# Kernel tuning notes

Measured on AMD Instinct MI355X. Metric: run time of the kernel, lower is better.

## Reference

```python
import jax, jax.numpy as jnp
import numpy as np

EMBED_DIM = 512
NUM_HEADS = 8
HEAD_DIM = EMBED_DIM // NUM_HEADS


def setup_inputs() -> dict:
    key = jax.random.key(0)
    k1, k2, kw, kb, kow, kob = jax.random.split(key, 6)
    B, L, C = 2, 2048, EMBED_DIM
    s = 1.0 / np.sqrt(C)
    return {
        "x1": jax.random.normal(k1, (B, L, C), dtype=jnp.float32),
        "x2": jax.random.normal(k2, (B, L, C), dtype=jnp.float32),
        # nn.Linear(embed_dim, 3*embed_dim): weight [3C, C], bias [3C]
        "qkv_w": jax.random.uniform(kw, (3 * C, C), jnp.float32, -s, s),
        "qkv_b": jax.random.uniform(kb, (3 * C,), jnp.float32, -s, s),
        # nn.Linear(embed_dim, embed_dim): weight [C, C], bias [C]
        "out_w": jax.random.uniform(kow, (C, C), jnp.float32, -s, s),
        "out_b": jax.random.uniform(kob, (C,), jnp.float32, -s, s),
    }


def _qkv(x, qkv_w, qkv_b):
    B, L, C = x.shape
    H, D = NUM_HEADS, C // NUM_HEADS
    # Linear: x @ W^T + b, then view(B, L, H, 3, D) and split along the '3' axis
    qkv = (jnp.einsum("blc,fc->blf", x, qkv_w) + qkv_b).reshape(B, L, H, 3, D)
    qkv = jnp.transpose(qkv, (3, 0, 2, 1, 4))  # [3, B, H, L, D]
    return qkv[0], qkv[1], qkv[2]


def _attend(q, k, v):
    # q,k,v: [B, H, L, D]; scale by 1/sqrt(D)
    scale = 1.0 / np.sqrt(q.shape[-1]).astype(np.float32)
    scores = jnp.einsum("bhqd,bhkd->bhqk", q, k) * scale  # [B,H,L,L]
    attn = jax.nn.softmax(scores, axis=-1)
    out = jnp.einsum("bhqk,bhkd->bhqd", attn, v)
    B, H, L, D = out.shape
    return jnp.transpose(out, (0, 2, 1, 3)).reshape(B, L, H * D)


def reference(x1, x2, qkv_w, qkv_b, out_w, out_b):
    q1, k1, v1 = _qkv(x1, qkv_w, qkv_b)
    q2, k2, v2 = _qkv(x2, qkv_w, qkv_b)
    out1 = _attend(q1, k2, v2)  # q from x1, k/v from x2
    out2 = _attend(q2, k1, v1)  # q from x2, k/v from x1
    out1 = jnp.einsum("blc,fc->blf", out1, out_w) + out_b
    out2 = jnp.einsum("blc,fc->blf", out2, out_w) + out_b
    return (out1, out2)
```

## Files before the change

kernel.cpp:

```cpp
#include <hip/hip_runtime.h>
#include <stdint.h>

typedef unsigned short u16;
typedef unsigned int u32;
typedef short bf16x8 __attribute__((ext_vector_type(8)));
typedef float f32x4 __attribute__((ext_vector_type(4)));
typedef float f32x16 __attribute__((ext_vector_type(16)));

#define K_DIM 512

__device__ __forceinline__ u16 f2bf(float f) {
  union { float f; u32 u; } v; v.f = f;
  return (u16)((v.u + 0x8000u) >> 16);
}
__device__ __forceinline__ u32 pk2(float lo, float hi) {
  union { float f; u32 u; } a, b; a.f = lo; b.f = hi;
  return __builtin_amdgcn_perm(b.u + 0x8000u, a.u + 0x8000u, 0x07060302u);
}

__global__ void cvt_kernel(const float* __restrict__ x1, const float* __restrict__ x2,
                           const float* __restrict__ qkvw, const float* __restrict__ outw,
                           u16* __restrict__ xb, u16* __restrict__ wqkv, u16* __restrict__ wout) {
  int tid = blockIdx.x * 256 + threadIdx.x;
  const float4* src; u16* dst; int idx = tid;
  if (idx < 524288)        { src = (const float4*)x1;   dst = xb; }
  else if (idx < 1048576)  { src = (const float4*)x2;   dst = xb + 2097152; idx -= 524288; }
  else if (idx < 1245184)  { src = (const float4*)qkvw; dst = wqkv;         idx -= 1048576; }
  else                     { src = (const float4*)outw; dst = wout;         idx -= 1245184; }
  float4 v = src[idx];
  *(uint2*)&dst[idx * 4] = make_uint2(pk2(v.x, v.y), pk2(v.z, v.w));
}

#define LDA 40

__global__ __launch_bounds__(256, 3) void qkv_gemm(
    const u16* __restrict__ A, const u16* __restrict__ W, const float* __restrict__ bias,
    u16* __restrict__ qb, u16* __restrict__ kb, u16* __restrict__ vtb) {
  __shared__ __align__(16) u16 As[2][128 * LDA];
  __shared__ __align__(16) u16 Bs[2][128 * LDA];
  const int t = threadIdx.x;
  const int m0 = blockIdx.x * 128, n0 = blockIdx.y * 128;
  const int lane = t & 63, l16 = lane & 15, quad = lane >> 4;
  const int w = t >> 6;
  const int wm = (w >> 1) * 64, wn = (w & 1) * 64;
  const int sr = t >> 2, sc = (t & 3) * 8;

  const u16* Ap = A + (size_t)(m0 + sr) * K_DIM + sc;
  const u16* Wp = W + (size_t)(n0 + sr) * K_DIM + sc;

  f32x4 acc[4][4];
#pragma unroll
  for (int i = 0; i < 4; ++i)
#pragma unroll
    for (int j = 0; j < 4; ++j) acc[i][j] = (f32x4){0.f, 0.f, 0.f, 0.f};

  uint4 ra0 = *(const uint4*)(Ap);
  uint4 ra1 = *(const uint4*)(Ap + 64 * K_DIM);
  uint4 rb0 = *(const uint4*)(Wp);
  uint4 rb1 = *(const uint4*)(Wp + 64 * K_DIM);
  *(uint4*)&As[0][sr * LDA + sc] = ra0;
  *(uint4*)&As[0][(sr + 64) * LDA + sc] = ra1;
  *(uint4*)&Bs[0][sr * LDA + sc] = rb0;
  *(uint4*)&Bs[0][(sr + 64) * LDA + sc] = rb1;
  ra0 = *(const uint4*)(Ap + 32);
  ra1 = *(const uint4*)(Ap + 64 * K_DIM + 32);
  rb0 = *(const uint4*)(Wp + 32);
  rb1 = *(const uint4*)(Wp + 64 * K_DIM + 32);
  __syncthreads();

  for (int kt = 0; kt < 16; ++kt) {
    const int cur = kt & 1, nxt = cur ^ 1;
    if (kt < 15) {
      *(uint4*)&As[nxt][sr * LDA + sc] = ra0;
      *(uint4*)&As[nxt][(sr + 64) * LDA + sc] = ra1;
      *(uint4*)&Bs[nxt][sr * LDA + sc] = rb0;
      *(uint4*)&Bs[nxt][(sr + 64) * LDA + sc] = rb1;
    }
    if (kt < 14) {
      int ko = (kt + 2) * 32;
      ra0 = *(const uint4*)(Ap + ko);
      ra1 = *(const uint4*)(Ap + 64 * K_DIM + ko);
      rb0 = *(const uint4*)(Wp + ko);
      rb1 = *(const uint4*)(Wp + 64 * K_DIM + ko);
    }
    bf16x8 af[4], bfr[4];
#pragma unroll
    for (int mi = 0; mi < 4; ++mi)
      af[mi] = *(const bf16x8*)&As[cur][(wm + mi * 16 + l16) * LDA + quad * 8];
#pragma unroll
    for (int ni = 0; ni < 4; ++ni)
      bfr[ni] = *(const bf16x8*)&Bs[cur][(wn + ni * 16 + l16) * LDA + quad * 8];
#pragma unroll
    for (int mi = 0; mi < 4; ++mi)
#pragma unroll
      for (int ni = 0; ni < 4; ++ni)
        acc[mi][ni] = __builtin_amdgcn_mfma_f32_16x16x32_bf16(bfr[ni], af[mi], acc[mi][ni], 0, 0, 0);
    __syncthreads();
  }

  const int fbase = n0 + wn;
  const int h = fbase / 192;
  const int s = (fbase - h * 192) >> 6;
  float4 bv[4];
#pragma unroll
  for (int ni = 0; ni < 4; ++ni)
    bv[ni] = *(const float4*)&bias[fbase + ni * 16 + quad * 4];
  const int bh = m0 >> 11;
  const int lbase = (m0 & 2047) + wm;

  if (s == 2) {
    u16* dst = vtb + (size_t)((bh * 8 + h) * 64) * 2048;
#pragma unroll
    for (int mi = 0; mi < 4; ++mi) {
      int l = lbase + mi * 16 + l16;
#pragma unroll
      for (int ni = 0; ni < 4; ++ni)
#pragma unroll
        for (int r = 0; r < 4; ++r)
          dst[(ni * 16 + quad * 4 + r) * 2048 + l] = f2bf(acc[mi][ni][r] + bv[ni][r]);
    }
  } else {
    u16* dst = (s == 0 ? qb : kb) + (size_t)((bh * 8 + h) * 2048) * 64;
    const float sc2 = (s == 0) ? 0.18033688011112042f : 1.0f;
#pragma unroll
    for (int mi = 0; mi < 4; ++mi) {
      int l = lbase + mi * 16 + l16;
#pragma unroll
      for (int ni = 0; ni < 4; ++ni) {
        float v0 = (acc[mi][ni][0] + bv[ni][0]) * sc2;
        float v1 = (acc[mi][ni][1] + bv[ni][1]) * sc2;
        float v2 = (acc[mi][ni][2] + bv[ni][2]) * sc2;
        float v3 = (acc[mi][ni][3] + bv[ni][3]) * sc2;
        *(uint2*)&dst[(size_t)l * 64 + ni * 16 + quad * 4] = make_uint2(pk2(v0, v1), pk2(v2, v3));
      }
    }
  }
}

#define LQ 72

#define SPHASE(SS, KBUF)                                                          \
  do {                                                                            \
    _Pragma("unroll") for (int r_ = 0; r_ < 16; ++r_) {                           \
      SS[0][r_] = 0.f; SS[1][r_] = 0.f;                                           \
    }                                                                             \
    _Pragma("unroll") for (int ks_ = 0; ks_ < 4; ++ks_) {                         \
      bf16x8 kfr0 = *(const bf16x8*)&Ks[KBUF][l32 * LQ + ks_ * 16 + h2 * 8];      \
      bf16x8 kfr1 = *(const bf16x8*)&Ks[KBUF][(32 + l32) * LQ + ks_ * 16 + h2 * 8]; \
      SS[0] = __builtin_amdgcn_mfma_f32_32x32x16_bf16(kfr0, qf[ks_], SS[0], 0, 0, 0); \
      SS[1] = __builtin_amdgcn_mfma_f32_32x32x16_bf16(kfr1, qf[ks_], SS[1], 0, 0, 0); \
    }                                                                             \
  } while (0)

#define SOFTPV(SS, VBUF)                                                          \
  do {                                                                            \
    bf16x8 pf[4];                                                                 \
    _Pragma("unroll") for (int mi_ = 0; mi_ < 2; ++mi_) {                         \
      float p[16];                                                                \
      _Pragma("unroll") for (int r_ = 0; r_ < 16; ++r_)                           \
        p[r_] = __builtin_amdgcn_exp2f(SS[mi_][r_]);                              \
      _Pragma("unroll") for (int r_ = 0; r_ < 16; r_ += 4)                        \
        rs += (p[r_] + p[r_ + 1]) + (p[r_ + 2] + p[r_ + 3]);                      \
      u32 a0 = pk2(p[0], p[1]),   b0 = pk2(p[2], p[3]);                           \
      u32 c0 = pk2(p[4], p[5]),   d0 = pk2(p[6], p[7]);                           \
      u32 a1 = pk2(p[8], p[9]),   b1 = pk2(p[10], p[11]);                         \
      u32 c1 = pk2(p[12], p[13]), d1 = pk2(p[14], p[15]);                         \
      asm("v_permlane32_swap_b32 %0, %1" : "+v"(a0), "+v"(c0));                   \
      asm("v_permlane32_swap_b32 %0, %1" : "+v"(b0), "+v"(d0));                   \
      asm("v_permlane32_swap_b32 %0, %1" : "+v"(a1), "+v"(c1));                   \
      asm("v_permlane32_swap_b32 %0, %1" : "+v"(b1), "+v"(d1));                   \
      union { u32 u[4]; bf16x8 v; } f0_, f1_;                                     \
      f0_.u[0] = a0; f0_.u[1] = b0; f0_.u[2] = c0; f0_.u[3] = d0;                 \
      f1_.u[0] = a1; f1_.u[1] = b1; f1_.u[2] = c1; f1_.u[3] = d1;                 \
      pf[mi_ * 2] = f0_.v; pf[mi_ * 2 + 1] = f1_.v;                               \
    }                                                                             \
    const u16* vb_ = (const u16*)VTs + (VBUF) * (64 * LQ);                        \
    _Pragma("unroll") for (int ks_ = 0; ks_ < 4; ++ks_) {                         \
      bf16x8 vf0 = *(const bf16x8*)&vb_[l32 * LQ + ks_ * 16 + h2 * 8];            \
      bf16x8 vf1 = *(const bf16x8*)&vb_[(32 + l32) * LQ + ks_ * 16 + h2 * 8];     \
      oacc[0] = __builtin_amdgcn_mfma_f32_32x32x16_bf16(vf0, pf[ks_], oacc[0], 0, 0, 0); \
      oacc[1] = __builtin_amdgcn_mfma_f32_32x32x16_bf16(vf1, pf[ks_], oacc[1], 0, 0, 0); \
    }                                                                             \
  } while (0)

__global__ __launch_bounds__(256, 2) void attn_kernel(
    const u16* __restrict__ qb, const u16* __restrict__ kb, const u16* __restrict__ vtb,
    u16* __restrict__ attnb) {
  __shared__ __align__(16) u16 Ks[2][64 * LQ];
  __shared__ __align__(16) u16 VTs[4][64 * LQ];

  const int t = threadIdx.x;
  const int w = t >> 6, lane = t & 63, l32 = lane & 31, h2 = lane >> 5;
  const int bid = blockIdx.x;
  const int comb = bid & 31;
  const int qt = bid >> 5;
  const int h = comb & 7, bb = (comb >> 3) & 1, pair = comb >> 4;
  const int in_q = pair, in_kv = pair ^ 1;

  const u16* Qg = qb + (size_t)((in_q * 2 + bb) * 8 + h) * 2048 * 64;
  const u16* Kg = kb + (size_t)((in_kv * 2 + bb) * 8 + h) * 2048 * 64;
  const u16* Vg = vtb + (size_t)((in_kv * 2 + bb) * 8 + h) * 64 * 2048;

  const int srow = t >> 3, sseg = (t & 7) * 8;
  uint4 rk0 = *(const uint4*)(Kg + srow * 64 + sseg);
  uint4 rk1 = *(const uint4*)(Kg + (srow + 32) * 64 + sseg);
  uint4 rv0 = *(const uint4*)(Vg + srow * 2048 + sseg);
  uint4 rv1 = *(const uint4*)(Vg + (srow + 32) * 2048 + sseg);

  bf16x8 qf[4];
#pragma unroll
  for (int ks = 0; ks < 4; ++ks)
    qf[ks] = *(const bf16x8*)(Qg + (qt * 128 + w * 32 + l32) * 64 + ks * 16 + h2 * 8);

  auto stage = [&](int kbuf, int vbuf) {
    *(uint4*)&Ks[kbuf][srow * LQ + sseg] = rk0;
    *(uint4*)&Ks[kbuf][(srow + 32) * LQ + sseg] = rk1;
    *(uint4*)&VTs[vbuf][srow * LQ + sseg] = rv0;
    *(uint4*)&VTs[vbuf][(srow + 32) * LQ + sseg] = rv1;
  };
  auto gload = [&](int kt) {
    const int ko = kt * 64;
    rk0 = *(const uint4*)(Kg + (ko + srow) * 64 + sseg);
    rk1 = *(const uint4*)(Kg + (ko + srow + 32) * 64 + sseg);
    rv0 = *(const uint4*)(Vg + srow * 2048 + ko + sseg);
    rv1 = *(const uint4*)(Vg + (srow + 32) * 2048 + ko + sseg);
  };

  f32x16 oacc[2];
#pragma unroll
  for (int mi = 0; mi < 2; ++mi)
#pragma unroll
    for (int r = 0; r < 16; ++r) oacc[mi][r] = 0.f;
  float rs = 0.f;
  f32x16 sA[2], sB[2];

  stage(0, 0);
  gload(1);
  __syncthreads();

  SPHASE(sA, 0);
  stage(1, 1);
  gload(2);
  __syncthreads();

#pragma unroll 1
  for (int it = 0; it < 16; ++it) {
    const int e = (it & 1) << 1;
    SPHASE(sB, 1);
    SOFTPV(sA, e);
    if (it == 15) break;
    stage(0, e ^ 2);
    gload(2 * it + 3);
    __syncthreads();
    SPHASE(sA, 0);
    SOFTPV(sB, e + 1);
    stage(1, e ^ 3);
    if (it < 14) gload(2 * it + 4);
    __syncthreads();
  }
  SOFTPV(sB, 3);

  rs += __shfl_xor(rs, 32);
  const float inv = 1.0f / rs;
  const int row = in_q * 4096 + bb * 2048 + qt * 128 + w * 32 + l32;
#pragma unroll
  for (int mi = 0; mi < 2; ++mi)
#pragma unroll
    for (int rg = 0; rg < 4; ++rg) {
      float v0 = oacc[mi][rg * 4 + 0] * inv;
      float v1 = oacc[mi][rg * 4 + 1] * inv;
      float v2 = oacc[mi][rg * 4 + 2] * inv;
      float v3 = oacc[mi][rg * 4 + 3] * inv;
      *(uint2*)&attnb[(size_t)row * 512 + h * 64 + mi * 32 + rg * 8 + h2 * 4] =
          make_uint2(pk2(v0, v1), pk2(v2, v3));
    }
}

__global__ __launch_bounds__(256, 2) void out_gemm(
    const u16* __restrict__ A, const u16* __restrict__ W, const float* __restrict__ bias,
    float* __restrict__ out) {
  __shared__ __align__(16) u16 As[2][64 * LDA];
  __shared__ __align__(16) u16 Bs[2][128 * LDA];
  const int t = threadIdx.x;
  const int m0 = blockIdx.x * 64, n0 = blockIdx.y * 128;
  const int lane = t & 63, l16 = lane & 15, quad = lane >> 4;
  const int w = t >> 6;
  const int wm = (w & 1) * 32, wn = (w >> 1) * 64;
  const int ar = t >> 2, ac = (t & 3) * 8;
  const int sr = t >> 2, sc = (t & 3) * 8;

  const u16* Ap = A + (size_t)(m0 + ar) * K_DIM + ac;
  const u16* Wp = W + (size_t)(n0 + sr) * K_DIM + sc;

  f32x4 acc[2][4];
#pragma unroll
  for (int i = 0; i < 2; ++i)
#pragma unroll
    for (int j = 0; j < 4; ++j) acc[i][j] = (f32x4){0.f, 0.f, 0.f, 0.f};

  uint4 ra = *(const uint4*)Ap;
  uint4 rb0 = *(const uint4*)(Wp);
  uint4 rb1 = *(const uint4*)(Wp + 64 * K_DIM);
  *(uint4*)&As[0][ar * LDA + ac] = ra;
  *(uint4*)&Bs[0][sr * LDA + sc] = rb0;
  *(uint4*)&Bs[0][(sr + 64) * LDA + sc] = rb1;
  ra = *(const uint4*)(Ap + 32);
  rb0 = *(const uint4*)(Wp + 32);
  rb1 = *(const uint4*)(Wp + 64 * K_DIM + 32);
  __syncthreads();

  for (int kt = 0; kt < 16; ++kt) {
    const int cur = kt & 1, nxt = cur ^ 1;
    if (kt < 15) {
      *(uint4*)&As[nxt][ar * LDA + ac] = ra;
      *(uint4*)&Bs[nxt][sr * LDA + sc] = rb0;
      *(uint4*)&Bs[nxt][(sr + 64) * LDA + sc] = rb1;
    }
    if (kt < 14) {
      int ko = (kt + 2) * 32;
      ra = *(const uint4*)(Ap + ko);
      rb0 = *(const uint4*)(Wp + ko);
      rb1 = *(const uint4*)(Wp + 64 * K_DIM + ko);
    }
    bf16x8 af[2], bfr[4];
#pragma unroll
    for (int mi = 0; mi < 2; ++mi)
      af[mi] = *(const bf16x8*)&As[cur][(wm + mi * 16 + l16) * LDA + quad * 8];
#pragma unroll
    for (int ni = 0; ni < 4; ++ni)
      bfr[ni] = *(const bf16x8*)&Bs[cur][(wn + ni * 16 + l16) * LDA + quad * 8];
#pragma unroll
    for (int mi = 0; mi < 2; ++mi)
#pragma unroll
      for (int ni = 0; ni < 4; ++ni)
        acc[mi][ni] = __builtin_amdgcn_mfma_f32_16x16x32_bf16(af[mi], bfr[ni], acc[mi][ni], 0, 0, 0);
    __syncthreads();
  }

#pragma unroll
  for (int ni = 0; ni < 4; ++ni) {
    int f = n0 + wn + ni * 16 + l16;
    float bv = bias[f];
#pragma unroll
    for (int mi = 0; mi < 2; ++mi)
#pragma unroll
      for (int r = 0; r < 4; ++r) {
        int m = m0 + wm + mi * 16 + quad * 4 + r;
        out[(size_t)m * 512 + f] = acc[mi][ni][r] + bv;
      }
  }
}

extern "C" void kernel_launch(void* const* d_in, const int* in_sizes, int n_in,
                              void* d_out, int out_size, void* d_ws, size_t ws_size,
                              hipStream_t stream) {
  const float* x1   = (const float*)d_in[0];
  const float* x2   = (const float*)d_in[1];
  const float* qkvw = (const float*)d_in[2];
  const float* qkvb = (const float*)d_in[3];
  const float* outw = (const float*)d_in[4];
  const float* outb = (const float*)d_in[5];
  float* out = (float*)d_out;
  char* ws = (char*)d_ws;

  u16* xb    = (u16*)(ws + 0);
  u16* wqkv  = (u16*)(ws + 8388608);
  u16* wout  = (u16*)(ws + 9961472);
  u16* qb    = (u16*)(ws + 10485760);
  u16* kb    = (u16*)(ws + 18874368);
  u16* vtb   = (u16*)(ws + 27262976);
  u16* attnb = (u16*)(ws + 0);

  cvt_kernel<<<5120, 256, 0, stream>>>(x1, x2, qkvw, outw, xb, wqkv, wout);

  dim3 g1(64, 12);
  qkv_gemm<<<g1, 256, 0, stream>>>(xb, wqkv, qkvb, qb, kb, vtb);

  attn_kernel<<<512, 256, 0, stream>>>(qb, kb, vtb, attnb);

  dim3 g3(128, 4);
  out_gemm<<<g3, 256, 0, stream>>>(attnb, wout, outb, out);
}
```

Baseline: 150.5 us.

## Split attention KV tile across two wave groups with LDS reduction

Doubles the attention block to 512 threads. Each 64-key tile is split so waves 0-3 handle the first 32 keys and waves 4-7 the second 32 for the same query rows. Partial output accumulators and row sums are combined through shared memory at the end. This halves per-wave MFMA and register work and spreads staging loads over more threads, aiming for more latency hiding and occupancy. In exchange it adds a final LDS reduction with extra barriers and duplicates the Q-fragment loads.

```diff
diff --git a/kernel.cpp b/kernel.cpp
--- a/kernel.cpp
+++ b/kernel.cpp
@@ -141,49 +141,44 @@
 
 #define SPHASE(SS, KBUF)                                                          \
   do {                                                                            \
-    _Pragma("unroll") for (int r_ = 0; r_ < 16; ++r_) {                           \
-      SS[0][r_] = 0.f; SS[1][r_] = 0.f;                                           \
-    }                                                                             \
+    _Pragma("unroll") for (int r_ = 0; r_ < 16; ++r_) SS[r_] = 0.f;               \
     _Pragma("unroll") for (int ks_ = 0; ks_ < 4; ++ks_) {                         \
-      bf16x8 kfr0 = *(const bf16x8*)&Ks[KBUF][l32 * LQ + ks_ * 16 + h2 * 8];      \
-      bf16x8 kfr1 = *(const bf16x8*)&Ks[KBUF][(32 + l32) * LQ + ks_ * 16 + h2 * 8]; \
-      SS[0] = __builtin_amdgcn_mfma_f32_32x32x16_bf16(kfr0, qf[ks_], SS[0], 0, 0, 0); \
-      SS[1] = __builtin_amdgcn_mfma_f32_32x32x16_bf16(kfr1, qf[ks_], SS[1], 0, 0, 0); \
+      bf16x8 kfr = *(const bf16x8*)&Ks[KBUF][(half32 + l32) * LQ + ks_ * 16 + h2 * 8]; \
+      SS = __builtin_amdgcn_mfma_f32_32x32x16_bf16(kfr, qf[ks_], SS, 0, 0, 0);    \
     }                                                                             \
   } while (0)
 
 #define SOFTPV(SS, VBUF)                                                          \
   do {                                                                            \
-    bf16x8 pf[4];                                                                 \
-    _Pragma("unroll") for (int mi_ = 0; mi_ < 2; ++mi_) {                         \
-      float p[16];                                                                \
-      _Pragma("unroll") for (int r_ = 0; r_ < 16; ++r_)                           \
-        p[r_] = __builtin_amdgcn_exp2f(SS[mi_][r_]);                              \
-      _Pragma("unroll") for (int r_ = 0; r_ < 16; r_ += 4)                        \
-        rs += (p[r_] + p[r_ + 1]) + (p[r_ + 2] + p[r_ + 3]);                      \
-      u32 a0 = pk2(p[0], p[1]),   b0 = pk2(p[2], p[3]);                           \
-      u32 c0 = pk2(p[4], p[5]),   d0 = pk2(p[6], p[7]);                           \
-      u32 a1 = pk2(p[8], p[9]),   b1 = pk2(p[10], p[11]);                         \
-      u32 c1 = pk2(p[12], p[13]), d1 = pk2(p[14], p[15]);                         \
-      asm("v_permlane32_swap_b32 %0, %1" : "+v"(a0), "+v"(c0));                   \
-      asm("v_permlane32_swap_b32 %0, %1" : "+v"(b0), "+v"(d0));                   \
-      asm("v_permlane32_swap_b32 %0, %1" : "+v"(a1), "+v"(c1));                   \
-      asm("v_permlane32_swap_b32 %0, %1" : "+v"(b1), "+v"(d1));                   \
-      union { u32 u[4]; bf16x8 v; } f0_, f1_;                                     \
-      f0_.u[0] = a0; f0_.u[1] = b0; f0_.u[2] = c0; f0_.u[3] = d0;                 \
-      f1_.u[0] = a1; f1_.u[1] = b1; f1_.u[2] = c1; f1_.u[3] = d1;                 \
-      pf[mi_ * 2] = f0_.v; pf[mi_ * 2 + 1] = f1_.v;                               \
-    }                                                                             \
+    float p[16];                                                                  \
+    _Pragma("unroll") for (int r_ = 0; r_ < 16; ++r_)                             \
+      p[r_] = __builtin_amdgcn_exp2f(SS[r_]);                                     \
+    _Pragma("unroll") for (int r_ = 0; r_ < 16; r_ += 4)                          \
+      rs += (p[r_] + p[r_ + 1]) + (p[r_ + 2] + p[r_ + 3]);                        \
+    u32 a0 = pk2(p[0], p[1]),   b0 = pk2(p[2], p[3]);                             \
+    u32 c0 = pk2(p[4], p[5]),   d0 = pk2(p[6], p[7]);                             \
+    u32 a1 = pk2(p[8], p[9]),   b1 = pk2(p[10], p[11]);                           \
+    u32 c1 = pk2(p[12], p[13]), d1 = pk2(p[14], p[15]);                           \
+    asm("v_permlane32_swap_b32 %0, %1" : "+v"(a0), "+v"(c0));                     \
+    asm("v_permlane32_swap_b32 %0, %1" : "+v"(b0), "+v"(d0));                     \
+    asm("v_permlane32_swap_b32 %0, %1" : "+v"(a1), "+v"(c1));                     \
+    asm("v_permlane32_swap_b32 %0, %1" : "+v"(b1), "+v"(d1));                     \
+    union { u32 u[4]; bf16x8 v; } f0_, f1_;                                       \
+    f0_.u[0] = a0; f0_.u[1] = b0; f0_.u[2] = c0; f0_.u[3] = d0;                   \
+    f1_.u[0] = a1; f1_.u[1] = b1; f1_.u[2] = c1; f1_.u[3] = d1;                   \
+    bf16x8 pf0 = f0_.v, pf1 = f1_.v;                                              \
     const u16* vb_ = (const u16*)VTs + (VBUF) * (64 * LQ);                        \
-    _Pragma("unroll") for (int ks_ = 0; ks_ < 4; ++ks_) {                         \
-      bf16x8 vf0 = *(const bf16x8*)&vb_[l32 * LQ + ks_ * 16 + h2 * 8];            \
-      bf16x8 vf1 = *(const bf16x8*)&vb_[(32 + l32) * LQ + ks_ * 16 + h2 * 8];     \
-      oacc[0] = __builtin_amdgcn_mfma_f32_32x32x16_bf16(vf0, pf[ks_], oacc[0], 0, 0, 0); \
-      oacc[1] = __builtin_amdgcn_mfma_f32_32x32x16_bf16(vf1, pf[ks_], oacc[1], 0, 0, 0); \
-    }                                                                             \
+    bf16x8 vf0 = *(const bf16x8*)&vb_[l32 * LQ + half32 + h2 * 8];                \
+    bf16x8 vf1 = *(const bf16x8*)&vb_[(32 + l32) * LQ + half32 + h2 * 8];         \
+    oacc[0] = __builtin_amdgcn_mfma_f32_32x32x16_bf16(vf0, pf0, oacc[0], 0, 0, 0);\
+    oacc[1] = __builtin_amdgcn_mfma_f32_32x32x16_bf16(vf1, pf0, oacc[1], 0, 0, 0);\
+    vf0 = *(const bf16x8*)&vb_[l32 * LQ + half32 + 16 + h2 * 8];                  \
+    vf1 = *(const bf16x8*)&vb_[(32 + l32) * LQ + half32 + 16 + h2 * 8];           \
+    oacc[0] = __builtin_amdgcn_mfma_f32_32x32x16_bf16(vf0, pf1, oacc[0], 0, 0, 0);\
+    oacc[1] = __builtin_amdgcn_mfma_f32_32x32x16_bf16(vf1, pf1, oacc[1], 0, 0, 0);\
   } while (0)
 
-__global__ __launch_bounds__(256, 2) void attn_kernel(
+__global__ __launch_bounds__(512, 4) void attn_kernel(
     const u16* __restrict__ qb, const u16* __restrict__ kb, const u16* __restrict__ vtb,
     u16* __restrict__ attnb) {
   __shared__ __align__(16) u16 Ks[2][64 * LQ];
@@ -191,6 +186,7 @@
 
   const int t = threadIdx.x;
   const int w = t >> 6, lane = t & 63, l32 = lane & 31, h2 = lane >> 5;
+  const int qg = w & 3, half32 = (w >> 2) * 32;
   const int bid = blockIdx.x;
   const int comb = bid & 31;
   const int qt = bid >> 5;
@@ -203,27 +199,21 @@
 
   const int srow = t >> 3, sseg = (t & 7) * 8;
   uint4 rk0 = *(const uint4*)(Kg + srow * 64 + sseg);
-  uint4 rk1 = *(const uint4*)(Kg + (srow + 32) * 64 + sseg);
   uint4 rv0 = *(const uint4*)(Vg + srow * 2048 + sseg);
-  uint4 rv1 = *(const uint4*)(Vg + (srow + 32) * 2048 + sseg);
 
   bf16x8 qf[4];
 #pragma unroll
   for (int ks = 0; ks < 4; ++ks)
-    qf[ks] = *(const bf16x8*)(Qg + (qt * 128 + w * 32 + l32) * 64 + ks * 16 + h2 * 8);
+    qf[ks] = *(const bf16x8*)(Qg + (qt * 128 + qg * 32 + l32) * 64 + ks * 16 + h2 * 8);
 
   auto stage = [&](int kbuf, int vbuf) {
     *(uint4*)&Ks[kbuf][srow * LQ + sseg] = rk0;
-    *(uint4*)&Ks[kbuf][(srow + 32) * LQ + sseg] = rk1;
     *(uint4*)&VTs[vbuf][srow * LQ + sseg] = rv0;
-    *(uint4*)&VTs[vbuf][(srow + 32) * LQ + sseg] = rv1;
   };
   auto gload = [&](int kt) {
     const int ko = kt * 64;
     rk0 = *(const uint4*)(Kg + (ko + srow) * 64 + sseg);
-    rk1 = *(const uint4*)(Kg + (ko + srow + 32) * 64 + sseg);
     rv0 = *(const uint4*)(Vg + srow * 2048 + ko + sseg);
-    rv1 = *(const uint4*)(Vg + (srow + 32) * 2048 + ko + sseg);
   };
 
   f32x16 oacc[2];
@@ -232,7 +222,7 @@
 #pragma unroll
     for (int r = 0; r < 16; ++r) oacc[mi][r] = 0.f;
   float rs = 0.f;
-  f32x16 sA[2], sB[2];
+  f32x16 sA, sB;
 
   stage(0, 0);
   gload(1);
@@ -261,19 +251,43 @@
   SOFTPV(sB, 3);
 
   rs += __shfl_xor(rs, 32);
-  const float inv = 1.0f / rs;
-  const int row = in_q * 4096 + bb * 2048 + qt * 128 + w * 32 + l32;
-#pragma unroll
-  for (int mi = 0; mi < 2; ++mi)
-#pragma unroll
-    for (int rg = 0; rg < 4; ++rg) {
-      float v0 = oacc[mi][rg * 4 + 0] * inv;
-      float v1 = oacc[mi][rg * 4 + 1] * inv;
-      float v2 = oacc[mi][rg * 4 + 2] * inv;
-      float v3 = oacc[mi][rg * 4 + 3] * inv;
-      *(uint2*)&attnb[(size_t)row * 512 + h * 64 + mi * 32 + rg * 8 + h2 * 4] =
-          make_uint2(pk2(v0, v1), pk2(v2, v3));
-    }
+  __syncthreads();
+  float* red = (float*)&VTs[0][0];
+  float* rsb = red + 4 * 64 * 32;
+  if (half32) {
+#pragma unroll
+    for (int mi = 0; mi < 2; ++mi)
+#pragma unroll
+      for (int r = 0; r < 16; ++r) {
+        int d = mi * 32 + (r & 3) + 8 * (r >> 2) + 4 * h2;
+        red[(qg * 64 + d) * 32 + l32] = oacc[mi][r];
+      }
+    if (lane < 32) rsb[qg * 32 + l32] = rs;
+  }
+  __syncthreads();
+  if (!half32) {
+#pragma unroll
+    for (int mi = 0; mi < 2; ++mi)
+#pragma unroll
+      for (int r = 0; r < 16; ++r) {
+        int d = mi * 32 + (r & 3) + 8 * (r >> 2) + 4 * h2;
+        oacc[mi][r] += red[(qg * 64 + d) * 32 + l32];
+      }
+    rs += rsb[qg * 32 + l32];
+    const float inv = 1.0f / rs;
+    const int row = in_q * 4096 + bb * 2048 + qt * 128 + qg * 32 + l32;
+#pragma unroll
+    for (int mi = 0; mi < 2; ++mi)
+#pragma unroll
+      for (int rg = 0; rg < 4; ++rg) {
+        float v0 = oacc[mi][rg * 4 + 0] * inv;
+        float v1 = oacc[mi][rg * 4 + 1] * inv;
+        float v2 = oacc[mi][rg * 4 + 2] * inv;
+        float v3 = oacc[mi][rg * 4 + 3] * inv;
+        *(uint2*)&attnb[(size_t)row * 512 + h * 64 + mi * 32 + rg * 8 + h2 * 4] =
+            make_uint2(pk2(v0, v1), pk2(v2, v3));
+      }
+  }
 }
 
 __global__ __launch_bounds__(256, 2) void out_gemm(
@@ -376,7 +390,7 @@
   dim3 g1(64, 12);
   qkv_gemm<<<g1, 256, 0, stream>>>(xb, wqkv, qkvb, qb, kb, vtb);
 
-  attn_kernel<<<512, 256, 0, stream>>>(qb, kb, vtb, attnb);
+  attn_kernel<<<512, 512, 0, stream>>>(qb, kb, vtb, attnb);
 
   dim3 g3(128, 4);
   out_gemm<<<g3, 256, 0, stream>>>(attnb, wout, outb, out);
```

New measurement: 158.6 us. 5.4% more time.
